# Optimization experiments

Hardware: AMD Instinct MI355X
Metric: run time of the kernel (lower is better)

Reference implementation:

```python
import jax, jax.numpy as jnp
import numpy as np

T = 512  # time_step

def setup_inputs() -> dict:
    key = jax.random.key(0)
    k1, k2, k3 = jax.random.split(key, 3)
    inputs = jax.random.normal(k1, (64, 1024, T), dtype=jnp.float32)
    # Dense stand-in for the ModuleList of Linear(i+1, 1): row i uses cols 0..i.
    # PyTorch Linear init scale ~ U(-1/sqrt(fan_in), 1/sqrt(fan_in)); simple normal is fine for a correctness baseline.
    W = jax.random.normal(k2, (T, T), dtype=jnp.float32) * 0.05
    b = jax.random.normal(k3, (T,), dtype=jnp.float32) * 0.05
    return {"inputs": inputs, "W": W, "b": b}

def reference(inputs, W, b):
    # out[..., i] = sum_{j<=i} inputs[..., j] * W[i, j] + b[i]
    Wtri = jnp.tril(W)  # lower-triangular mask == prefix Linear structure
    return jnp.einsum('bnj,ij->bni', inputs, Wtri) + b
```

## Files before the change

kernel.cpp:

```cpp
#include <hip/hip_runtime.h>
#include <hip/hip_bf16.h>


#define TK 512
#define BM 128
#define BN 128
#define BK 64

typedef __attribute__((ext_vector_type(4))) float f32x4;
typedef __attribute__((ext_vector_type(8))) __bf16 bf16x8;

__global__ __launch_bounds__(256, 2)
void triu_gemm_kernel(const float* __restrict__ X, const float* __restrict__ W,
                      const float* __restrict__ bias, float* __restrict__ out) {
    const int bm = blockIdx.x * BM;
    const int n0 = blockIdx.y * BN;
    const int kmax = n0 + BN;

    __shared__ __bf16 As[BM][BK];
    __shared__ __bf16 Bs[BN][BK];

    const int t    = threadIdx.x;
    const int wave = t >> 6;
    const int lane = t & 63;
    const int wr   = wave >> 1;
    const int wc   = wave & 1;
    const int l15  = lane & 15;
    const int l4   = lane >> 4;

    const int srow   = t >> 3;
    const int schunk = t & 7;

    f32x4 acc[4][4];
    #pragma unroll
    for (int m = 0; m < 4; ++m)
        #pragma unroll
        for (int n = 0; n < 4; ++n)
            acc[m][n] = (f32x4){0.f, 0.f, 0.f, 0.f};

    for (int k0 = 0; k0 < kmax; k0 += BK) {
        __syncthreads();

        #pragma unroll
        for (int i = 0; i < 4; ++i) {
            const int row = i * 32 + srow;
            const float* src = X + (size_t)(bm + row) * TK + k0 + schunk * 8;
            f32x4 v0 = *reinterpret_cast<const f32x4*>(src);
            f32x4 v1 = *reinterpret_cast<const f32x4*>(src + 4);
            bf16x8 p;
            p[0] = (__bf16)v0[0]; p[1] = (__bf16)v0[1];
            p[2] = (__bf16)v0[2]; p[3] = (__bf16)v0[3];
            p[4] = (__bf16)v1[0]; p[5] = (__bf16)v1[1];
            p[6] = (__bf16)v1[2]; p[7] = (__bf16)v1[3];
            const int wchunk = schunk ^ (row & 7);
            *reinterpret_cast<bf16x8*>(&As[row][wchunk * 8]) = p;
        }

        #pragma unroll
        for (int i = 0; i < 4; ++i) {
            const int row  = i * 32 + srow;
            const int ncol = n0 + row;
            const float* src = W + (size_t)ncol * TK + k0 + schunk * 8;
            f32x4 v0 = *reinterpret_cast<const f32x4*>(src);
            f32x4 v1 = *reinterpret_cast<const f32x4*>(src + 4);
            const int kbase = k0 + schunk * 8;
            bf16x8 p;
            #pragma unroll
            for (int e = 0; e < 4; ++e)
                p[e] = (kbase + e <= ncol) ? (__bf16)v0[e] : (__bf16)0.f;
            #pragma unroll
            for (int e = 0; e < 4; ++e)
                p[4 + e] = (kbase + 4 + e <= ncol) ? (__bf16)v1[e] : (__bf16)0.f;
            const int wchunk = schunk ^ (row & 7);
            *reinterpret_cast<bf16x8*>(&Bs[row][wchunk * 8]) = p;
        }

        __syncthreads();

        #pragma unroll
        for (int ks = 0; ks < 2; ++ks) {
            bf16x8 a[4], bb[4];
            #pragma unroll
            for (int m = 0; m < 4; ++m) {
                const int row    = wr * 64 + m * 16 + l15;
                const int chunk  = ks * 4 + l4;
                const int rchunk = chunk ^ (row & 7);
                a[m] = *reinterpret_cast<const bf16x8*>(&As[row][rchunk * 8]);
            }
            #pragma unroll
            for (int n = 0; n < 4; ++n) {
                const int row    = wc * 64 + n * 16 + l15;
                const int chunk  = ks * 4 + l4;
                const int rchunk = chunk ^ (row & 7);
                bb[n] = *reinterpret_cast<const bf16x8*>(&Bs[row][rchunk * 8]);
            }
            #pragma unroll
            for (int m = 0; m < 4; ++m)
                #pragma unroll
                for (int n = 0; n < 4; ++n)
                    acc[m][n] = __builtin_amdgcn_mfma_f32_16x16x32_bf16(
                        a[m], bb[n], acc[m][n], 0, 0, 0);
        }
    }

    #pragma unroll
    for (int n = 0; n < 4; ++n) {
        const int col = n0 + wc * 64 + n * 16 + l15;
        const float bv = bias[col];
        #pragma unroll
        for (int m = 0; m < 4; ++m) {
            const int row0 = bm + wr * 64 + m * 16 + l4 * 4;
            #pragma unroll
            for (int j = 0; j < 4; ++j)
                out[(size_t)(row0 + j) * TK + col] = acc[m][n][j] + bv;
        }
    }
}

extern "C" void kernel_launch(void* const* d_in, const int* in_sizes, int n_in,
                              void* d_out, int out_size, void* d_ws, size_t ws_size,
                              hipStream_t stream) {
    const float* X = (const float*)d_in[0];
    const float* W = (const float*)d_in[1];
    const float* b = (const float*)d_in[2];
    float* out = (float*)d_out;

    const int M = in_sizes[0] / TK;
    dim3 grid(M / BM, TK / BN);
    triu_gemm_kernel<<<grid, 256, 0, stream>>>(X, W, b, out);
}
```

Before: 269.3 us.

## Prefetch next K tile into registers while computing current tile

Splits the tile staging into a global-load phase that fills registers and a convert-and-store phase that writes to shared memory. The loop now issues the next tile's global loads before the MFMA work on the current tile, then converts and writes them after a barrier. This is meant to hide global-memory latency behind compute. In exchange it raises register pressure with 16 extra float4 values per thread, which could hurt occupancy under launch_bounds(256,2).

```diff
diff --git a/kernel.cpp b/kernel.cpp
--- a/kernel.cpp
+++ b/kernel.cpp
@@ -38,44 +38,54 @@
         for (int n = 0; n < 4; ++n)
             acc[m][n] = (f32x4){0.f, 0.f, 0.f, 0.f};
 
-    for (int k0 = 0; k0 < kmax; k0 += BK) {
-        __syncthreads();
+    f32x4 pa[4][2], pb[4][2];
 
+    auto issue_loads = [&](int k0) {
         #pragma unroll
         for (int i = 0; i < 4; ++i) {
             const int row = i * 32 + srow;
-            const float* src = X + (size_t)(bm + row) * TK + k0 + schunk * 8;
-            f32x4 v0 = *reinterpret_cast<const f32x4*>(src);
-            f32x4 v1 = *reinterpret_cast<const f32x4*>(src + 4);
-            bf16x8 p;
-            p[0] = (__bf16)v0[0]; p[1] = (__bf16)v0[1];
-            p[2] = (__bf16)v0[2]; p[3] = (__bf16)v0[3];
-            p[4] = (__bf16)v1[0]; p[5] = (__bf16)v1[1];
-            p[6] = (__bf16)v1[2]; p[7] = (__bf16)v1[3];
-            const int wchunk = schunk ^ (row & 7);
-            *reinterpret_cast<bf16x8*>(&As[row][wchunk * 8]) = p;
+            const float* sa = X + (size_t)(bm + row) * TK + k0 + schunk * 8;
+            pa[i][0] = *reinterpret_cast<const f32x4*>(sa);
+            pa[i][1] = *reinterpret_cast<const f32x4*>(sa + 4);
+            const float* sb = W + (size_t)(n0 + row) * TK + k0 + schunk * 8;
+            pb[i][0] = *reinterpret_cast<const f32x4*>(sb);
+            pb[i][1] = *reinterpret_cast<const f32x4*>(sb + 4);
         }
+    };
 
+    auto write_tiles = [&](int k0) {
+        const int kbase = k0 + schunk * 8;
         #pragma unroll
         for (int i = 0; i < 4; ++i) {
-            const int row  = i * 32 + srow;
-            const int ncol = n0 + row;
-            const float* src = W + (size_t)ncol * TK + k0 + schunk * 8;
-            f32x4 v0 = *reinterpret_cast<const f32x4*>(src);
-            f32x4 v1 = *reinterpret_cast<const f32x4*>(src + 4);
-            const int kbase = k0 + schunk * 8;
+            const int row    = i * 32 + srow;
+            const int wchunk = schunk ^ (row & 7);
             bf16x8 p;
             #pragma unroll
-            for (int e = 0; e < 4; ++e)
-                p[e] = (kbase + e <= ncol) ? (__bf16)v0[e] : (__bf16)0.f;
+            for (int e = 0; e < 4; ++e) p[e]     = (__bf16)pa[i][0][e];
+            #pragma unroll
+            for (int e = 0; e < 4; ++e) p[4 + e] = (__bf16)pa[i][1][e];
+            *reinterpret_cast<bf16x8*>(&As[row][wchunk * 8]) = p;
+
+            const int ncol = n0 + row;
+            bf16x8 q;
             #pragma unroll
             for (int e = 0; e < 4; ++e)
-                p[4 + e] = (kbase + 4 + e <= ncol) ? (__bf16)v1[e] : (__bf16)0.f;
-            const int wchunk = schunk ^ (row & 7);
-            *reinterpret_cast<bf16x8*>(&Bs[row][wchunk * 8]) = p;
+                q[e]     = (kbase + e     <= ncol) ? (__bf16)pb[i][0][e] : (__bf16)0.f;
+            #pragma unroll
+            for (int e = 0; e < 4; ++e)
+                q[4 + e] = (kbase + 4 + e <= ncol) ? (__bf16)pb[i][1][e] : (__bf16)0.f;
+            *reinterpret_cast<bf16x8*>(&Bs[row][wchunk * 8]) = q;
         }
+    };
 
-        __syncthreads();
+    issue_loads(0);
+    write_tiles(0);
+    __syncthreads();
+
+    for (int k0 = 0; k0 < kmax; k0 += BK) {
+        const int kn = k0 + BK;
+        const bool has_next = kn < kmax;
+        if (has_next) issue_loads(kn);
 
         #pragma unroll
         for (int ks = 0; ks < 2; ++ks) {
@@ -83,15 +93,13 @@
             #pragma unroll
             for (int m = 0; m < 4; ++m) {
                 const int row    = wr * 64 + m * 16 + l15;
-                const int chunk  = ks * 4 + l4;
-                const int rchunk = chunk ^ (row & 7);
+                const int rchunk = (ks * 4 + l4) ^ (row & 7);
                 a[m] = *reinterpret_cast<const bf16x8*>(&As[row][rchunk * 8]);
             }
             #pragma unroll
             for (int n = 0; n < 4; ++n) {
                 const int row    = wc * 64 + n * 16 + l15;
-                const int chunk  = ks * 4 + l4;
-                const int rchunk = chunk ^ (row & 7);
+                const int rchunk = (ks * 4 + l4) ^ (row & 7);
                 bb[n] = *reinterpret_cast<const bf16x8*>(&Bs[row][rchunk * 8]);
             }
             #pragma unroll
@@ -101,6 +109,10 @@
                     acc[m][n] = __builtin_amdgcn_mfma_f32_16x16x32_bf16(
                         a[m], bb[n], acc[m][n], 0, 0, 0);
         }
+
+        __syncthreads();
+        if (has_next) write_tiles(kn);
+        __syncthreads();
     }
 
     #pragma unroll
```

After: 264.8 us. Within noise of the previous version (-1.7%).

## Drop shared-memory staging; load operands directly to registers with pre-masked bf16 W

Applied to the files above, without the earlier changes.

Adds a prep kernel that converts W to bf16 and applies the lower-triangular mask once into the workspace. The GEMM kernel no longer uses LDS or barriers: each wave loads its MFMA fragments straight from global memory, with X converted to bf16 in registers. Occupancy is raised to 3 blocks per CU. The aim is to remove LDS round trips and syncs, at the cost of redundant global/L2 reads of X and W across waves and an extra kernel launch.

```diff
diff --git a/kernel.cpp b/kernel.cpp
--- a/kernel.cpp
+++ b/kernel.cpp
@@ -5,20 +5,30 @@
 #define TK 512
 #define BM 128
 #define BN 128
-#define BK 64
 
 typedef __attribute__((ext_vector_type(4))) float f32x4;
+typedef __attribute__((ext_vector_type(4))) __bf16 bf16x4;
 typedef __attribute__((ext_vector_type(8))) __bf16 bf16x8;
 
-__global__ __launch_bounds__(256, 2)
-void triu_gemm_kernel(const float* __restrict__ X, const float* __restrict__ W,
+__global__ __launch_bounds__(256)
+void prep_w_kernel(const float* __restrict__ W, __bf16* __restrict__ Wb) {
+    const int tid = blockIdx.x * 256 + threadIdx.x;
+    const int i  = tid >> 7;
+    const int j0 = (tid & 127) * 4;
+    f32x4 v = *reinterpret_cast<const f32x4*>(W + (size_t)i * TK + j0);
+    bf16x4 o;
+    #pragma unroll
+    for (int e = 0; e < 4; ++e)
+        o[e] = (j0 + e <= i) ? (__bf16)v[e] : (__bf16)0.f;
+    *reinterpret_cast<bf16x4*>(Wb + (size_t)i * TK + j0) = o;
+}
+
+__global__ __launch_bounds__(256, 3)
+void triu_gemm_kernel(const float* __restrict__ X, const __bf16* __restrict__ Wb,
                       const float* __restrict__ bias, float* __restrict__ out) {
     const int bm = blockIdx.x * BM;
     const int n0 = blockIdx.y * BN;
     const int kmax = n0 + BN;
-
-    __shared__ __bf16 As[BM][BK];
-    __shared__ __bf16 Bs[BN][BK];
 
     const int t    = threadIdx.x;
     const int wave = t >> 6;
@@ -28,8 +38,14 @@
     const int l15  = lane & 15;
     const int l4   = lane >> 4;
 
-    const int srow   = t >> 3;
-    const int schunk = t & 7;
+    const float*  xb[4];
+    const __bf16* wb[4];
+    #pragma unroll
+    for (int m = 0; m < 4; ++m)
+        xb[m] = X + (size_t)(bm + wr * 64 + m * 16 + l15) * TK + l4 * 8;
+    #pragma unroll
+    for (int n = 0; n < 4; ++n)
+        wb[n] = Wb + (size_t)(n0 + wc * 64 + n * 16 + l15) * TK + l4 * 8;
 
     f32x4 acc[4][4];
     #pragma unroll
@@ -38,69 +54,28 @@
         for (int n = 0; n < 4; ++n)
             acc[m][n] = (f32x4){0.f, 0.f, 0.f, 0.f};
 
-    for (int k0 = 0; k0 < kmax; k0 += BK) {
-        __syncthreads();
+    #pragma unroll 2
+    for (int kk = 0; kk < kmax; kk += 32) {
+        bf16x8 a[4], b[4];
+        #pragma unroll
+        for (int m = 0; m < 4; ++m) {
+            f32x4 v0 = *reinterpret_cast<const f32x4*>(xb[m] + kk);
+            f32x4 v1 = *reinterpret_cast<const f32x4*>(xb[m] + kk + 4);
+            #pragma unroll
+            for (int e = 0; e < 4; ++e) a[m][e]     = (__bf16)v0[e];
+            #pragma unroll
+            for (int e = 0; e < 4; ++e) a[m][4 + e] = (__bf16)v1[e];
+        }
+        #pragma unroll
+        for (int n = 0; n < 4; ++n)
+            b[n] = *reinterpret_cast<const bf16x8*>(wb[n] + kk);
 
         #pragma unroll
-        for (int i = 0; i < 4; ++i) {
-            const int row = i * 32 + srow;
-            const float* src = X + (size_t)(bm + row) * TK + k0 + schunk * 8;
-            f32x4 v0 = *reinterpret_cast<const f32x4*>(src);
-            f32x4 v1 = *reinterpret_cast<const f32x4*>(src + 4);
-            bf16x8 p;
-            p[0] = (__bf16)v0[0]; p[1] = (__bf16)v0[1];
-            p[2] = (__bf16)v0[2]; p[3] = (__bf16)v0[3];
-            p[4] = (__bf16)v1[0]; p[5] = (__bf16)v1[1];
-            p[6] = (__bf16)v1[2]; p[7] = (__bf16)v1[3];
-            const int wchunk = schunk ^ (row & 7);
-            *reinterpret_cast<bf16x8*>(&As[row][wchunk * 8]) = p;
-        }
-
-        #pragma unroll
-        for (int i = 0; i < 4; ++i) {
-            const int row  = i * 32 + srow;
-            const int ncol = n0 + row;
-            const float* src = W + (size_t)ncol * TK + k0 + schunk * 8;
-            f32x4 v0 = *reinterpret_cast<const f32x4*>(src);
-            f32x4 v1 = *reinterpret_cast<const f32x4*>(src + 4);
-            const int kbase = k0 + schunk * 8;
-            bf16x8 p;
+        for (int m = 0; m < 4; ++m)
             #pragma unroll
-            for (int e = 0; e < 4; ++e)
-                p[e] = (kbase + e <= ncol) ? (__bf16)v0[e] : (__bf16)0.f;
-            #pragma unroll
-            for (int e = 0; e < 4; ++e)
-                p[4 + e] = (kbase + 4 + e <= ncol) ? (__bf16)v1[e] : (__bf16)0.f;
-            const int wchunk = schunk ^ (row & 7);
-            *reinterpret_cast<bf16x8*>(&Bs[row][wchunk * 8]) = p;
-        }
-
-        __syncthreads();
-
-        #pragma unroll
-        for (int ks = 0; ks < 2; ++ks) {
-            bf16x8 a[4], bb[4];
-            #pragma unroll
-            for (int m = 0; m < 4; ++m) {
-                const int row    = wr * 64 + m * 16 + l15;
-                const int chunk  = ks * 4 + l4;
-                const int rchunk = chunk ^ (row & 7);
-                a[m] = *reinterpret_cast<const bf16x8*>(&As[row][rchunk * 8]);
-            }
-            #pragma unroll
-            for (int n = 0; n < 4; ++n) {
-                const int row    = wc * 64 + n * 16 + l15;
-                const int chunk  = ks * 4 + l4;
-                const int rchunk = chunk ^ (row & 7);
-                bb[n] = *reinterpret_cast<const bf16x8*>(&Bs[row][rchunk * 8]);
-            }
-            #pragma unroll
-            for (int m = 0; m < 4; ++m)
-                #pragma unroll
-                for (int n = 0; n < 4; ++n)
-                    acc[m][n] = __builtin_amdgcn_mfma_f32_16x16x32_bf16(
-                        a[m], bb[n], acc[m][n], 0, 0, 0);
-        }
+            for (int n = 0; n < 4; ++n)
+                acc[m][n] = __builtin_amdgcn_mfma_f32_16x16x32_bf16(
+                    a[m], b[n], acc[m][n], 0, 0, 0);
     }
 
     #pragma unroll
@@ -124,8 +99,11 @@
     const float* W = (const float*)d_in[1];
     const float* b = (const float*)d_in[2];
     float* out = (float*)d_out;
+    __bf16* Wb = (__bf16*)d_ws;
+
+    prep_w_kernel<<<256, 256, 0, stream>>>(W, Wb);
 
     const int M = in_sizes[0] / TK;
     dim3 grid(M / BM, TK / BN);
-    triu_gemm_kernel<<<grid, 256, 0, stream>>>(X, W, b, out);
+    triu_gemm_kernel<<<grid, 256, 0, stream>>>(X, Wb, b, out);
 }
```

Result: slower. 330.1 us (+22.6%).
